# Kernel tuning notes

Measured on AMD Instinct MI355X. Metric: run time of the kernel, lower is better.

Reference implementation:

```python
import jax, jax.numpy as jnp
import numpy as np


def dequant_weight(cb, idx):
    """Reconstruct weight from product-quantization codebooks.
    cb:  [C, K, sub]  codebooks
    idx: [C, out]     int codes per codebook per output row
    returns W: [out, C*sub]
    """
    C = cb.shape[0]
    gathered = cb[jnp.arange(C)[:, None], idx]          # [C, out, sub]
    W = jnp.transpose(gathered, (1, 0, 2))               # [out, C, sub]
    return W.reshape(W.shape[0], -1)                     # [out, C*sub]


def setup_inputs() -> dict:
    key = jax.random.key(0)
    ks = jax.random.split(key, 7)
    B, S, D, H, C, K = 4, 2048, 1024, 4096, 8, 256
    return {
        "x": jax.random.normal(ks[0], (B, S, D), dtype=jnp.float32),
        "cb1": jax.random.normal(ks[1], (C, K, D // C), dtype=jnp.float32) * 0.02,
        "idx1": jax.random.randint(ks[2], (C, H), 0, K, dtype=jnp.int32),
        "b1": jax.random.normal(ks[3], (H,), dtype=jnp.float32) * 0.02,
        "cb2": jax.random.normal(ks[4], (C, K, H // C), dtype=jnp.float32) * 0.02,
        "idx2": jax.random.randint(ks[5], (C, D), 0, K, dtype=jnp.int32),
        "b2": jax.random.normal(ks[6], (D,), dtype=jnp.float32) * 0.02,
    }


def reference(x, cb1, idx1, b1, cb2, idx2, b2):
    # fc1: dequantize W1 [hidden, dim] from shared codebooks, then linear
    W1 = dequant_weight(cb1, idx1)                       # [H, D]
    h = jnp.einsum("bsd,hd->bsh", x, W1) + b1            # [B, S, H]
    h = jax.nn.gelu(h, approximate=False)                # exact GELU (torch default)
    # fc2: dequantize W2 [dim, hidden], linear back to dim
    W2 = dequant_weight(cb2, idx2)                       # [D, H]
    return jnp.einsum("bsh,dh->bsd", h, W2) + b2         # [B, S, D]
```

## Files before the change

kernel.cpp:

```cpp
#include <hip/hip_runtime.h>
#include <hip/hip_bf16.h>
#include <math.h>

typedef __bf16 bf16_t;
typedef bf16_t bf16x8 __attribute__((ext_vector_type(8)));
typedef float f32x4 __attribute__((ext_vector_type(4)));

__device__ __forceinline__ void g2l16(const bf16_t* g, bf16_t* l) {
    __builtin_amdgcn_global_load_lds(
        (const __attribute__((address_space(1))) void*)g,
        (__attribute__((address_space(3))) void*)l, 16, 0, 0);
}

__global__ void prep_all(const void* __restrict__ x,
                         const void* __restrict__ cb1, const int* __restrict__ idx1,
                         const void* __restrict__ b1,
                         const void* __restrict__ cb2, const int* __restrict__ idx2,
                         const void* __restrict__ b2,
                         bf16_t* __restrict__ xb, bf16_t* __restrict__ w1b,
                         bf16_t* __restrict__ w2b, float* __restrict__ b1f,
                         float* __restrict__ b2f, int* __restrict__ flag, int M) {
    __shared__ int s_bad;
    if (threadIdx.x == 0) s_bad = 0;
    __syncthreads();
    const unsigned short* xu = (const unsigned short*)x;
    int cnt = 0;
    for (int i = threadIdx.x; i < 8192; i += 256)
        cnt += (((xu[i] >> 7) & 0xFF) >= 0x88);
#pragma unroll
    for (int o = 32; o > 0; o >>= 1) cnt += __shfl_down(cnt, o, 64);
    if ((threadIdx.x & 63) == 0) atomicAdd(&s_bad, cnt);
    __syncthreads();
    const int f32 = (s_bad > 4);
    if (blockIdx.x == 0 && threadIdx.x == 0) flag[0] = f32;

    const int T0 = (M * 1024) / 8;
    const int T1 = 4096 * 128;
    const int T2 = 1024 * 512;
    const int TB = (4096 + 1024) / 8;
    const int total = T0 + T1 + T2 + TB;
    const int t = blockIdx.x * 256 + threadIdx.x;
    const int stride = gridDim.x * 256;

    for (int i = t; i < total; i += stride) {
        if (i < T0) {
            bf16x8 o;
            if (f32) {
                const float4* p = (const float4*)x;
                float4 a = p[2 * i], b = p[2 * i + 1];
                o[0] = (bf16_t)a.x; o[1] = (bf16_t)a.y; o[2] = (bf16_t)a.z; o[3] = (bf16_t)a.w;
                o[4] = (bf16_t)b.x; o[5] = (bf16_t)b.y; o[6] = (bf16_t)b.z; o[7] = (bf16_t)b.w;
            } else {
                o = ((const bf16x8*)x)[i];
            }
            *(bf16x8*)(xb + (size_t)i * 8) = o;
        } else if (i < T0 + T1 + T2) {
            int g2 = (i >= T0 + T1);
            int ii = g2 ? (i - T0 - T1) : (i - T0);
            int rows = g2 ? 1024 : 4096;
            int logsub = g2 ? 9 : 7;
            int sub = 1 << logsub;
            const int* idx = g2 ? idx2 : idx1;
            const void* cb = g2 ? cb2 : cb1;
            bf16_t* W = g2 ? w2b : w1b;
            int r = ii >> logsub;
            int col = (ii & (sub - 1)) << 3;
            int c = col >> logsub;
            int j = col & (sub - 1);
            int code = idx[c * rows + r];
            size_t src = ((size_t)(c * 256 + code) << logsub) + j;
            bf16x8 o;
            if (f32) {
                const float* s = (const float*)cb + src;
                float4 a = *(const float4*)s;
                float4 b = *(const float4*)(s + 4);
                o[0] = (bf16_t)a.x; o[1] = (bf16_t)a.y; o[2] = (bf16_t)a.z; o[3] = (bf16_t)a.w;
                o[4] = (bf16_t)b.x; o[5] = (bf16_t)b.y; o[6] = (bf16_t)b.z; o[7] = (bf16_t)b.w;
            } else {
                o = *(const bf16x8*)((const bf16_t*)cb + src);
            }
            *(bf16x8*)(W + (size_t)r * ((size_t)sub << 3) + col) = o;
        } else {
            int g = i - (T0 + T1 + T2);
#pragma unroll
            for (int j = 0; j < 8; ++j) {
                int e = g * 8 + j;
                float v;
                const void* src = (e < 4096) ? b1 : b2;
                int k = (e < 4096) ? e : e - 4096;
                v = f32 ? ((const float*)src)[k] : (float)(((const bf16_t*)src)[k]);
                if (e < 4096) b1f[k] = v; else b2f[k] = v;
            }
        }
    }
}

template <bool XCDSW, bool GELU, bool DYNOUT>
__global__ __launch_bounds__(256, 2)
void gemm_bt(const bf16_t* __restrict__ A, const bf16_t* __restrict__ Bw,
             const float* __restrict__ bias,
             bf16_t* __restrict__ obf, float* __restrict__ of32,
             int M, int N, int K, const int* __restrict__ flag) {
    __shared__ __attribute__((aligned(16))) bf16_t sA[128 * 64];
    __shared__ __attribute__((aligned(16))) bf16_t sB[128 * 64];

    const int tid = threadIdx.x;

    int bm, bn;
    if (XCDSW) {
        const int l = blockIdx.y * gridDim.x + blockIdx.x;
        const int xcd = l & 7;
        const int i = l >> 3;
        const int per = gridDim.y >> 3;
        bm = (xcd * per + (i % per)) << 7;
        bn = (i / per) << 7;
    } else {
        bm = blockIdx.y << 7;
        bn = blockIdx.x << 7;
    }

    const int row0 = tid >> 3;
    const int kc0 = ((tid & 7) - row0) & 7;
    const bf16_t* gA = A + (size_t)(bm + row0) * K + kc0 * 8;
    const bf16_t* gB = Bw + (size_t)(bn + row0) * K + kc0 * 8;
    bf16_t* lA = sA + tid * 8;
    bf16_t* lB = sB + tid * 8;
    const size_t pskip = (size_t)32 * K;

    const int lane = tid & 63;
    const int wave = tid >> 6;
    const int quad = lane >> 4;
    const int lr = lane & 15;
    const int wm = (wave & 1) << 6;
    const int wn = (wave >> 1) << 6;

    const int arow = wm + lr;
    const int brow = wn + lr;
    const bf16x8* pA0 = (const bf16x8*)(sA + arow * 64 + ((quad + arow) & 7) * 8);
    const bf16x8* pA1 = (const bf16x8*)(sA + arow * 64 + ((quad + 4 + arow) & 7) * 8);
    const bf16x8* pB0 = (const bf16x8*)(sB + brow * 64 + ((quad + brow) & 7) * 8);
    const bf16x8* pB1 = (const bf16x8*)(sB + brow * 64 + ((quad + 4 + brow) & 7) * 8);

    f32x4 acc[4][4] = {};

    for (int k0 = 0; k0 < K; k0 += 64) {
#pragma unroll
        for (int p = 0; p < 4; ++p) g2l16(gA + p * pskip + k0, lA + p * 2048);
#pragma unroll
        for (int p = 0; p < 4; ++p) g2l16(gB + p * pskip + k0, lB + p * 2048);
        __syncthreads();

        bf16x8 af[4], bf[4];
#pragma unroll
        for (int f = 0; f < 4; ++f) { af[f] = pA0[f * 128]; bf[f] = pB0[f * 128]; }
#pragma unroll
        for (int mi = 0; mi < 4; ++mi)
#pragma unroll
            for (int ni = 0; ni < 4; ++ni)
                acc[mi][ni] = __builtin_amdgcn_mfma_f32_16x16x32_bf16(
                    af[mi], bf[ni], acc[mi][ni], 0, 0, 0);
#pragma unroll
        for (int f = 0; f < 4; ++f) { af[f] = pA1[f * 128]; bf[f] = pB1[f * 128]; }
#pragma unroll
        for (int mi = 0; mi < 4; ++mi)
#pragma unroll
            for (int ni = 0; ni < 4; ++ni)
                acc[mi][ni] = __builtin_amdgcn_mfma_f32_16x16x32_bf16(
                    af[mi], bf[ni], acc[mi][ni], 0, 0, 0);
        __syncthreads();
    }

    const int outf32 = DYNOUT ? *flag : 0;
#pragma unroll
    for (int mi = 0; mi < 4; ++mi) {
#pragma unroll
        for (int ni = 0; ni < 4; ++ni) {
            const int n = bn + wn + ni * 16 + lr;
            const float bs = bias[n];
            f32x4 v = acc[mi][ni];
#pragma unroll
            for (int r = 0; r < 4; ++r) {
                const int m = bm + wm + mi * 16 + quad * 4 + r;
                float val = v[r] + bs;
                if (GELU) val = 0.5f * val * (1.0f + erff(val * 0.70710678118654752f));
                const size_t o = (size_t)m * N + n;
                if (DYNOUT) {
                    if (outf32) of32[o] = val;
                    else        obf[o] = (bf16_t)val;
                } else {
                    obf[o] = (bf16_t)val;
                }
            }
        }
    }
}

template <bool GELU, bool DYNOUT>
__global__ __launch_bounds__(512, 2)
void gemm256(const bf16_t* __restrict__ A, const bf16_t* __restrict__ Bw,
             const float* __restrict__ bias,
             bf16_t* __restrict__ obf, float* __restrict__ of32,
             int M, int N, int K, const int* __restrict__ flag) {
    __shared__ __attribute__((aligned(16))) bf16_t sA[2 * 256 * 64];
    __shared__ __attribute__((aligned(16))) bf16_t sB[2 * 256 * 64];

    const int tid = threadIdx.x;
    const int NT = K >> 6;

    const int l = blockIdx.x;
    const int nbm = M >> 8;
    const int per = nbm >> 3;
    const int xcd = l & 7;
    const int i = l >> 3;
    const int bm = (xcd * per + (i % per)) << 8;
    const int bn = (i / per) << 8;

    const int row0 = tid >> 3;
    const int kc = ((tid & 7) - row0) & 7;
    const bf16_t* gA0 = A + (size_t)(bm + row0) * K + kc * 8;
    const bf16_t* gB0 = Bw + (size_t)(bn + row0) * K + kc * 8;
    bf16_t* lA0 = sA + tid * 8;
    bf16_t* lB0 = sB + tid * 8;

#define STAGE_A(off_, h_, kt_) do {                                   \
    const bf16_t* g_ = gA0 + (size_t)((h_) * 128) * K + (kt_) * 64;   \
    bf16_t* l_ = lA0 + (off_) + (h_) * 8192;                          \
    g2l16(g_, l_);                                                    \
    g2l16(g_ + (size_t)64 * K, l_ + 4096);                            \
} while (0)
#define STAGE_B(off_, h_, kt_) do {                                   \
    const bf16_t* g_ = gB0 + (size_t)((h_) * 128) * K + (kt_) * 64;   \
    bf16_t* l_ = lB0 + (off_) + (h_) * 8192;                          \
    g2l16(g_, l_);                                                    \
    g2l16(g_ + (size_t)64 * K, l_ + 4096);                            \
} while (0)

    const int lane = tid & 63;
    const int wave = tid >> 6;
    const int wm = wave >> 2;
    const int wn = wave & 3;
    const int lr = lane & 15;
    const int quad = lane >> 4;
    const int c0 = ((quad + lr) & 7) * 8;
    const int c1 = ((quad + lr + 4) & 7) * 8;
    const bf16_t* pA = sA + (wm * 128 + lr) * 64;
    const bf16_t* pB = sB + (wn * 64 + lr) * 64;

    f32x4 acc[8][4] = {};
    bf16x8 afr[8][2], bfr[2][2];

    STAGE_A(0, 0, 0); STAGE_A(0, 1, 0); STAGE_B(0, 0, 0); STAGE_B(0, 1, 0);
    if (NT > 1) { STAGE_A(16384, 0, 1); STAGE_A(16384, 1, 1); STAGE_B(16384, 0, 1); }
    asm volatile("s_waitcnt vmcnt(6)" ::: "memory");
    __builtin_amdgcn_s_barrier();

    for (int t = 0; t < NT; ++t) {
        const int bo = (t & 1) << 14;
        const int obo = bo ^ 16384;

#pragma unroll
        for (int mi = 0; mi < 8; ++mi) {
            afr[mi][0] = *(const bf16x8*)(pA + bo + mi * 1024 + c0);
            afr[mi][1] = *(const bf16x8*)(pA + bo + mi * 1024 + c1);
        }
#pragma unroll
        for (int j = 0; j < 2; ++j) {
            bfr[j][0] = *(const bf16x8*)(pB + bo + j * 1024 + c0);
            bfr[j][1] = *(const bf16x8*)(pB + bo + j * 1024 + c1);
        }
        if (t + 1 < NT) STAGE_B(obo, 1, t + 1);
        __builtin_amdgcn_s_barrier();
        asm volatile("s_waitcnt lgkmcnt(0)");
        __builtin_amdgcn_s_setprio(1);
#pragma unroll
        for (int mi = 0; mi < 4; ++mi)
#pragma unroll
            for (int j = 0; j < 2; ++j) {
                acc[mi][j] = __builtin_amdgcn_mfma_f32_16x16x32_bf16(
                    afr[mi][0], bfr[j][0], acc[mi][j], 0, 0, 0);
                acc[mi][j] = __builtin_amdgcn_mfma_f32_16x16x32_bf16(
                    afr[mi][1], bfr[j][1], acc[mi][j], 0, 0, 0);
            }
        __builtin_amdgcn_s_setprio(0);
        __builtin_amdgcn_s_barrier();

        if (t + 2 < NT) STAGE_A(bo, 0, t + 2);
        __builtin_amdgcn_s_barrier();
        __builtin_amdgcn_s_setprio(1);
#pragma unroll
        for (int mi = 4; mi < 8; ++mi)
#pragma unroll
            for (int j = 0; j < 2; ++j) {
                acc[mi][j] = __builtin_amdgcn_mfma_f32_16x16x32_bf16(
                    afr[mi][0], bfr[j][0], acc[mi][j], 0, 0, 0);
                acc[mi][j] = __builtin_amdgcn_mfma_f32_16x16x32_bf16(
                    afr[mi][1], bfr[j][1], acc[mi][j], 0, 0, 0);
            }
        __builtin_amdgcn_s_setprio(0);
        __builtin_amdgcn_s_barrier();

#pragma unroll
        for (int j = 0; j < 2; ++j) {
            bfr[j][0] = *(const bf16x8*)(pB + bo + (2 + j) * 1024 + c0);
            bfr[j][1] = *(const bf16x8*)(pB + bo + (2 + j) * 1024 + c1);
        }
        if (t + 2 < NT) STAGE_A(bo, 1, t + 2);
        __builtin_amdgcn_s_barrier();
        asm volatile("s_waitcnt lgkmcnt(0)");
        __builtin_amdgcn_s_setprio(1);
#pragma unroll
        for (int mi = 4; mi < 8; ++mi)
#pragma unroll
            for (int j = 0; j < 2; ++j) {
                acc[mi][2 + j] = __builtin_amdgcn_mfma_f32_16x16x32_bf16(
                    afr[mi][0], bfr[j][0], acc[mi][2 + j], 0, 0, 0);
                acc[mi][2 + j] = __builtin_amdgcn_mfma_f32_16x16x32_bf16(
                    afr[mi][1], bfr[j][1], acc[mi][2 + j], 0, 0, 0);
            }
        __builtin_amdgcn_s_setprio(0);
        __builtin_amdgcn_s_barrier();

        if (t + 2 < NT) STAGE_B(bo, 0, t + 2);
        __builtin_amdgcn_s_barrier();
        __builtin_amdgcn_s_setprio(1);
#pragma unroll
        for (int mi = 0; mi < 4; ++mi)
#pragma unroll
            for (int j = 0; j < 2; ++j) {
                acc[mi][2 + j] = __builtin_amdgcn_mfma_f32_16x16x32_bf16(
                    afr[mi][0], bfr[j][0], acc[mi][2 + j], 0, 0, 0);
                acc[mi][2 + j] = __builtin_amdgcn_mfma_f32_16x16x32_bf16(
                    afr[mi][1], bfr[j][1], acc[mi][2 + j], 0, 0, 0);
            }
        __builtin_amdgcn_s_setprio(0);
        if (t + 2 < NT) asm volatile("s_waitcnt vmcnt(6)" ::: "memory");
        else            asm volatile("s_waitcnt vmcnt(0)" ::: "memory");
        __builtin_amdgcn_s_barrier();
    }

#undef STAGE_A
#undef STAGE_B

    const int outf32 = DYNOUT ? *flag : 0;
    const int mrow = bm + wm * 128 + quad * 4;
    const int ncol = bn + wn * 64 + lr;
#pragma unroll
    for (int mi = 0; mi < 8; ++mi) {
#pragma unroll
        for (int j = 0; j < 4; ++j) {
            const int n = ncol + j * 16;
            const float bs = bias[n];
            f32x4 v = acc[mi][j];
#pragma unroll
            for (int r = 0; r < 4; ++r) {
                const int m = mrow + mi * 16 + r;
                float val = v[r] + bs;
                if (GELU) val = 0.5f * val * (1.0f + erff(val * 0.70710678118654752f));
                const size_t o = (size_t)m * N + n;
                if (DYNOUT) {
                    if (outf32) of32[o] = val;
                    else        obf[o] = (bf16_t)val;
                } else {
                    obf[o] = (bf16_t)val;
                }
            }
        }
    }
}

extern "C" void kernel_launch(void* const* d_in, const int* in_sizes, int n_in,
                              void* d_out, int out_size, void* d_ws, size_t ws_size,
                              hipStream_t stream) {
    const void* x   = d_in[0];
    const void* cb1 = d_in[1];
    const int*  idx1 = (const int*)d_in[2];
    const void* b1  = d_in[3];
    const void* cb2 = d_in[4];
    const int*  idx2 = (const int*)d_in[5];
    const void* b2  = d_in[6];

    const int D = 1024, H = 4096;
    const int M = in_sizes[0] / D;

    char* ws = (char*)d_ws;
    bf16_t* xb  = (bf16_t*)ws;
    bf16_t* w1b = (bf16_t*)(ws + (size_t)M * D * 2);
    bf16_t* hb  = (bf16_t*)((char*)w1b + (size_t)H * D * 2);
    bf16_t* w2b = (bf16_t*)((char*)hb + (size_t)M * H * 2);
    float*  b1f = (float*)((char*)w2b + (size_t)D * H * 2);
    float*  b2f = b1f + H;
    int*    flag = (int*)(b2f + D);

    prep_all<<<2048, 256, 0, stream>>>(x, cb1, idx1, b1, cb2, idx2, b2,
                                       xb, w1b, w2b, b1f, b2f, flag, M);

    gemm256<true, false><<<(M / 256) * (H / 256), 512, 0, stream>>>(
        xb, w1b, b1f, hb, nullptr, M, H, D, flag);

    dim3 g2(D / 128, M / 128);
    gemm_bt<true, false, true><<<g2, 256, 0, stream>>>(hb, w2b, b2f,
        (bf16_t*)d_out, (float*)d_out, M, D, H, flag);
}
```

Before: 267.2 us.

## Halve A-fragment registers and simplify to single-stage-ahead prefetch

Shrinks the A-fragment register array from 8 to 4 rows by reloading A fragments from LDS twice per K-tile. This cuts VGPR pressure and may allow higher occupancy. It also replaces the staggered two-tiles-ahead global-to-LDS schedule with one that issues all loads for the next tile at the start of each iteration and waits on vmcnt(0) at the end. The price is more LDS reads and less latency hiding of global loads, since prefetch depth drops from roughly two tiles to one.

```diff
diff --git a/kernel.cpp b/kernel.cpp
--- a/kernel.cpp
+++ b/kernel.cpp
@@ -247,54 +247,62 @@
     const bf16_t* pB = sB + (wn * 64 + lr) * 64;
 
     f32x4 acc[8][4] = {};
-    bf16x8 afr[8][2], bfr[2][2];
+    bf16x8 af[4][2], bfr[2][2];
 
     STAGE_A(0, 0, 0); STAGE_A(0, 1, 0); STAGE_B(0, 0, 0); STAGE_B(0, 1, 0);
-    if (NT > 1) { STAGE_A(16384, 0, 1); STAGE_A(16384, 1, 1); STAGE_B(16384, 0, 1); }
-    asm volatile("s_waitcnt vmcnt(6)" ::: "memory");
+    asm volatile("s_waitcnt vmcnt(0)" ::: "memory");
     __builtin_amdgcn_s_barrier();
 
     for (int t = 0; t < NT; ++t) {
         const int bo = (t & 1) << 14;
         const int obo = bo ^ 16384;
-
-#pragma unroll
-        for (int mi = 0; mi < 8; ++mi) {
-            afr[mi][0] = *(const bf16x8*)(pA + bo + mi * 1024 + c0);
-            afr[mi][1] = *(const bf16x8*)(pA + bo + mi * 1024 + c1);
+        const bool st = (t + 1 < NT);
+
+#pragma unroll
+        for (int mi = 0; mi < 4; ++mi) {
+            af[mi][0] = *(const bf16x8*)(pA + bo + mi * 1024 + c0);
+            af[mi][1] = *(const bf16x8*)(pA + bo + mi * 1024 + c1);
         }
 #pragma unroll
         for (int j = 0; j < 2; ++j) {
             bfr[j][0] = *(const bf16x8*)(pB + bo + j * 1024 + c0);
             bfr[j][1] = *(const bf16x8*)(pB + bo + j * 1024 + c1);
         }
-        if (t + 1 < NT) STAGE_B(obo, 1, t + 1);
-        __builtin_amdgcn_s_barrier();
-        asm volatile("s_waitcnt lgkmcnt(0)");
+        if (st) {
+            STAGE_A(obo, 0, t + 1); STAGE_A(obo, 1, t + 1);
+            STAGE_B(obo, 0, t + 1); STAGE_B(obo, 1, t + 1);
+        }
+        __builtin_amdgcn_s_barrier();
+        asm volatile("s_waitcnt lgkmcnt(0)" ::: "memory");
         __builtin_amdgcn_s_setprio(1);
 #pragma unroll
         for (int mi = 0; mi < 4; ++mi)
 #pragma unroll
             for (int j = 0; j < 2; ++j) {
                 acc[mi][j] = __builtin_amdgcn_mfma_f32_16x16x32_bf16(
-                    afr[mi][0], bfr[j][0], acc[mi][j], 0, 0, 0);
+                    af[mi][0], bfr[j][0], acc[mi][j], 0, 0, 0);
                 acc[mi][j] = __builtin_amdgcn_mfma_f32_16x16x32_bf16(
-                    afr[mi][1], bfr[j][1], acc[mi][j], 0, 0, 0);
+                    af[mi][1], bfr[j][1], acc[mi][j], 0, 0, 0);
             }
         __builtin_amdgcn_s_setprio(0);
         __builtin_amdgcn_s_barrier();
 
-        if (t + 2 < NT) STAGE_A(bo, 0, t + 2);
-        __builtin_amdgcn_s_barrier();
+#pragma unroll
+        for (int mi = 0; mi < 4; ++mi) {
+            af[mi][0] = *(const bf16x8*)(pA + bo + (4 + mi) * 1024 + c0);
+            af[mi][1] = *(const bf16x8*)(pA + bo + (4 + mi) * 1024 + c1);
+        }
+        __builtin_amdgcn_s_barrier();
+        asm volatile("s_waitcnt lgkmcnt(0)" ::: "memory");
         __builtin_amdgcn_s_setprio(1);
 #pragma unroll
-        for (int mi = 4; mi < 8; ++mi)
+        for (int mi = 0; mi < 4; ++mi)
 #pragma unroll
             for (int j = 0; j < 2; ++j) {
-                acc[mi][j] = __builtin_amdgcn_mfma_f32_16x16x32_bf16(
-                    afr[mi][0], bfr[j][0], acc[mi][j], 0, 0, 0);
-                acc[mi][j] = __builtin_amdgcn_mfma_f32_16x16x32_bf16(
-                    afr[mi][1], bfr[j][1], acc[mi][j], 0, 0, 0);
+                acc[4 + mi][j] = __builtin_amdgcn_mfma_f32_16x16x32_bf16(
+                    af[mi][0], bfr[j][0], acc[4 + mi][j], 0, 0, 0);
+                acc[4 + mi][j] = __builtin_amdgcn_mfma_f32_16x16x32_bf16(
+                    af[mi][1], bfr[j][1], acc[4 + mi][j], 0, 0, 0);
             }
         __builtin_amdgcn_s_setprio(0);
         __builtin_amdgcn_s_barrier();
@@ -304,37 +312,40 @@
             bfr[j][0] = *(const bf16x8*)(pB + bo + (2 + j) * 1024 + c0);
             bfr[j][1] = *(const bf16x8*)(pB + bo + (2 + j) * 1024 + c1);
         }
-        if (t + 2 < NT) STAGE_A(bo, 1, t + 2);
-        __builtin_amdgcn_s_barrier();
-        asm volatile("s_waitcnt lgkmcnt(0)");
+        __builtin_amdgcn_s_barrier();
+        asm volatile("s_waitcnt lgkmcnt(0)" ::: "memory");
         __builtin_amdgcn_s_setprio(1);
 #pragma unroll
-        for (int mi = 4; mi < 8; ++mi)
+        for (int mi = 0; mi < 4; ++mi)
+#pragma unroll
+            for (int j = 0; j < 2; ++j) {
+                acc[4 + mi][2 + j] = __builtin_amdgcn_mfma_f32_16x16x32_bf16(
+                    af[mi][0], bfr[j][0], acc[4 + mi][2 + j], 0, 0, 0);
+                acc[4 + mi][2 + j] = __builtin_amdgcn_mfma_f32_16x16x32_bf16(
+                    af[mi][1], bfr[j][1], acc[4 + mi][2 + j], 0, 0, 0);
+            }
+        __builtin_amdgcn_s_setprio(0);
+        __builtin_amdgcn_s_barrier();
+
+#pragma unroll
+        for (int mi = 0; mi < 4; ++mi) {
+            af[mi][0] = *(const bf16x8*)(pA + bo + mi * 1024 + c0);
+            af[mi][1] = *(const bf16x8*)(pA + bo + mi * 1024 + c1);
+        }
+        __builtin_amdgcn_s_barrier();
+        asm volatile("s_waitcnt lgkmcnt(0)" ::: "memory");
+        __builtin_amdgcn_s_setprio(1);
+#pragma unroll
+        for (int mi = 0; mi < 4; ++mi)
 #pragma unroll
             for (int j = 0; j < 2; ++j) {
                 acc[mi][2 + j] = __builtin_amdgcn_mfma_f32_16x16x32_bf16(
-                    afr[mi][0], bfr[j][0], acc[mi][2 + j], 0, 0, 0);
+                    af[mi][0], bfr[j][0], acc[mi][2 + j], 0, 0, 0);
                 acc[mi][2 + j] = __builtin_amdgcn_mfma_f32_16x16x32_bf16(
-                    afr[mi][1], bfr[j][1], acc[mi][2 + j], 0, 0, 0);
+                    af[mi][1], bfr[j][1], acc[mi][2 + j], 0, 0, 0);
             }
         __builtin_amdgcn_s_setprio(0);
-        __builtin_amdgcn_s_barrier();
-
-        if (t + 2 < NT) STAGE_B(bo, 0, t + 2);
-        __builtin_amdgcn_s_barrier();
-        __builtin_amdgcn_s_setprio(1);
-#pragma unroll
-        for (int mi = 0; mi < 4; ++mi)
-#pragma unroll
-            for (int j = 0; j < 2; ++j) {
-                acc[mi][2 + j] = __builtin_amdgcn_mfma_f32_16x16x32_bf16(
-                    afr[mi][0], bfr[j][0], acc[mi][2 + j], 0, 0, 0);
-                acc[mi][2 + j] = __builtin_amdgcn_mfma_f32_16x16x32_bf16(
-                    afr[mi][1], bfr[j][1], acc[mi][2 + j], 0, 0, 0);
-            }
-        __builtin_amdgcn_s_setprio(0);
-        if (t + 2 < NT) asm volatile("s_waitcnt vmcnt(6)" ::: "memory");
-        else            asm volatile("s_waitcnt vmcnt(0)" ::: "memory");
+        asm volatile("s_waitcnt vmcnt(0)" ::: "memory");
         __builtin_amdgcn_s_barrier();
     }
 
```

Result: no change. 271.9 us (+1.8%).
